# Kernel tuning notes

Hardware: AMD Instinct MI355X
Metric: run time of the kernel (lower is better)

The kernel has to match this reference:

```python
import jax, jax.numpy as jnp
import numpy as np
from jax import lax

N, IN_CH, FEAT, OUT_CH, H, W = 8, 3, 64, 3, 256, 256
EPS = 1e-8


def lrelu(x):
    return jnp.where(x >= 0, x, 0.2 * x)


def conv2d(x, w, b, stride, pad):
    y = lax.conv_general_dilated(x, w, (stride, stride), [(pad, pad), (pad, pad)],
                                 dimension_numbers=('NCHW', 'OIHW', 'NCHW'))
    return y + b[None, :, None, None]


def make_blur_kernel():
    # _make_kernel([1,3,3,1]): outer product, normalized
    k = jnp.array([1.0, 3.0, 3.0, 1.0], jnp.float32)
    k = k[None, :] * k[:, None]
    return k / k.sum()


def blur(x, kernel, pad):
    # upfirdn2d with up=down=1: pad then FIR-convolve (true convolution -> flip kernel)
    n, c, h, w = x.shape
    k = jnp.flip(kernel, (0, 1))[None, None]  # [1,1,kh,kw]
    y = lax.conv_general_dilated(x.reshape(n * c, 1, h, w), k, (1, 1),
                                 [(pad[0], pad[1]), (pad[0], pad[1])],
                                 dimension_numbers=('NCHW', 'OIHW', 'NCHW'))
    return y.reshape(n, c, y.shape[-2], y.shape[-1])


def mod_conv(x, s, w, swW, swb, sbW, sbb, mode, blur_k, activate=True):
    # x [n,c,h,w]; s [n,feat]; w [out,c,k,k]; style 1x1 convs on [n,feat,1,1] == matmuls
    kk = w.shape[-1]
    sw = lrelu(s @ swW.T + swb)                    # [n, c]  (style_weight)
    sb = lrelu(s @ sbW.T + sbb)                    # [n, out] (style_bias)
    weight = w[None] * sw[:, None, :, None, None]  # [n,out,c,k,k]
    d = lax.rsqrt(jnp.sum(weight * weight, axis=(2, 3, 4)) + EPS)
    weight = weight * d[:, :, None, None, None]    # demodulate
    if mode == 'up':
        # conv_transpose2d(stride=2, pad=0) == conv with lhs_dilation=2, pad k-1, flipped kernel
        wf = jnp.flip(weight, (-2, -1))
        def f(xi, wi):
            return lax.conv_general_dilated(xi[None], wi, (1, 1),
                    [(kk - 1, kk - 1)] * 2, lhs_dilation=(2, 2),
                    dimension_numbers=('NCHW', 'OIHW', 'NCHW'))[0]
        y = jax.vmap(f)(x, wf)
        y = blur(y, blur_k * 4.0, (1, 1))          # Blur(pad=(1,1), upsample_factor=2)
    elif mode == 'down':
        xb = blur(x, blur_k, (2, 2))               # Blur(pad=(2,2))
        def f(xi, wi):
            return lax.conv_general_dilated(xi[None], wi, (2, 2), [(0, 0)] * 2,
                    dimension_numbers=('NCHW', 'OIHW', 'NCHW'))[0]
        y = jax.vmap(f)(xb, weight)
    else:
        p = kk // 2
        def f(xi, wi):
            return lax.conv_general_dilated(xi[None], wi, (1, 1), [(p, p)] * 2,
                    dimension_numbers=('NCHW', 'OIHW', 'NCHW'))[0]
        y = jax.vmap(f)(x, weight)
    y = y + sb[:, :, None, None]
    return lrelu(y) if activate else y


def da_forward(x, ref, g0_w, g0_b, gr_w, gr_b,
               c0_w, c0_swW, c0_swb, c0_sbW, c0_sbb,
               mid_w, mid_swW, mid_swb, mid_sbW, mid_sbb,
               c6_w, c6_swW, c6_swb, c6_sbW, c6_sbb):
    bk = make_blur_kernel()
    # guide_net: conv s1/lrelu, conv s2/lrelu, conv s1/lrelu, conv s2/lrelu, conv s1, avgpool(1)
    h = lrelu(conv2d(ref, g0_w, g0_b, 1, 1))
    strides = (2, 1, 2, 1)
    for i in range(4):
        h = conv2d(h, gr_w[i], gr_b[i], strides[i], 1)
        if i < 3:
            h = lrelu(h)
    s = jnp.mean(h, axis=(2, 3))  # [n, feat]; AdaptiveAvgPool2d(1)

    mids = lambda i: (mid_w[i], mid_swW[i], mid_swb[i], mid_sbW[i], mid_sbb[i])
    f0 = mod_conv(x, s, c0_w, c0_swW, c0_swb, c0_sbW, c0_sbb, 'none', bk)
    f1 = mod_conv(f0, s, *mids(0), 'down', bk)
    f1 = mod_conv(f1, s, *mids(1), 'none', bk)
    f2 = mod_conv(f1, s, *mids(2), 'down', bk)
    f2 = mod_conv(f2, s, *mids(3), 'none', bk)
    f3 = mod_conv(f2, s, *mids(4), 'none', bk)
    f3 = mod_conv(f3, s, *mids(5), 'none', bk)
    f4 = mod_conv(f3 + f2, s, *mids(6), 'up', bk)
    f4 = mod_conv(f4, s, *mids(7), 'none', bk)
    f5 = mod_conv(f4 + f1, s, *mids(8), 'up', bk)
    f5 = mod_conv(f5, s, *mids(9), 'none', bk)
    out = mod_conv(f5 + f0, s, c6_w, c6_swW, c6_swb, c6_sbW, c6_sbb, 'none', bk, activate=False)
    return out


def setup_inputs() -> dict:
    key = jax.random.key(0)
    ks = jax.random.split(key, 24)
    f = FEAT
    inv = 1.0 / np.sqrt(f)
    d = {
        'x':   jax.random.normal(ks[0], (N, IN_CH, H, W), jnp.float32),
        'ref': jax.random.normal(ks[1], (N, IN_CH, H, W), jnp.float32),
        'g0_w': jax.random.normal(ks[2], (f, IN_CH, 3, 3), jnp.float32) * (1.0 / np.sqrt(IN_CH * 9)),
        'g0_b': jnp.zeros((f,), jnp.float32),
        'gr_w': jax.random.normal(ks[3], (4, f, f, 3, 3), jnp.float32) * (1.0 / np.sqrt(f * 9)),
        'gr_b': jnp.zeros((4, f), jnp.float32),
        'c0_w':   jax.random.normal(ks[4], (f, IN_CH, 3, 3), jnp.float32),
        'c0_swW': jax.random.normal(ks[5], (IN_CH, f), jnp.float32) * inv,
        'c0_swb': jnp.zeros((IN_CH,), jnp.float32),
        'c0_sbW': jax.random.normal(ks[6], (f, f), jnp.float32) * inv,
        'c0_sbb': jnp.zeros((f,), jnp.float32),
        'mid_w':   jax.random.normal(ks[7], (10, f, f, 3, 3), jnp.float32),
        'mid_swW': jax.random.normal(ks[8], (10, f, f), jnp.float32) * inv,
        'mid_swb': jnp.zeros((10, f), jnp.float32),
        'mid_sbW': jax.random.normal(ks[9], (10, f, f), jnp.float32) * inv,
        'mid_sbb': jnp.zeros((10, f), jnp.float32),
        'c6_w':   jax.random.normal(ks[10], (OUT_CH, f, 3, 3), jnp.float32),
        'c6_swW': jax.random.normal(ks[11], (f, f), jnp.float32) * inv,
        'c6_swb': jnp.zeros((f,), jnp.float32),
        'c6_sbW': jax.random.normal(ks[12], (OUT_CH, f), jnp.float32) * inv,
        'c6_sbb': jnp.zeros((OUT_CH,), jnp.float32),
    }
    return d


def reference(x, ref, g0_w, g0_b, gr_w, gr_b,
              c0_w, c0_swW, c0_swb, c0_sbW, c0_sbb,
              mid_w, mid_swW, mid_swb, mid_sbW, mid_sbb,
              c6_w, c6_swW, c6_swb, c6_sbW, c6_sbb):
    return da_forward(x, ref, g0_w, g0_b, gr_w, gr_b,
                      c0_w, c0_swW, c0_swb, c0_sbW, c0_sbb,
                      mid_w, mid_swW, mid_swb, mid_sbW, mid_sbb,
                      c6_w, c6_swW, c6_swb, c6_sbW, c6_sbb)
```

## Files before the change

kernel.cpp:

```cpp
#include <hip/hip_runtime.h>

#define LRELU(v) ((v) >= 0.f ? (v) : 0.2f * (v))

template<int S>
__global__ void conv64_gemm(const float* __restrict__ in, const float* __restrict__ Wt,
                            const float* __restrict__ bias, float* __restrict__ out,
                            int Hin, int Win, int Hout, int Wout, int pad, int act, int tilesX,
                            long long inStr, long long wStr, long long bStr, long long outStr)
{
    constexpr int CC  = (S == 1) ? 8 : 4;
    constexpr int TIN = (S == 1) ? 18 : 33;
    constexpr int RS  = (S == 1) ? 20 : 36;
    constexpr int NF4 = (S == 1) ? 3 : 5;
    constexpr int PW  = NF4 * 4;
    extern __shared__ float lds[];
    float* it = lds;
    float* wl = lds + CC * TIN * RS;

    int s = blockIdx.y;
    in   += (size_t)s * inStr;
    Wt   += (size_t)s * wStr;
    bias += (size_t)s * bStr;
    out  += (size_t)s * outStr;

    int b  = blockIdx.x;
    int tx = b % tilesX, ty = b / tilesX;
    int t  = threadIdx.x;
    int og = t >> 5;
    int pg = t & 31;
    int r  = pg >> 1, ch = pg & 1;

    float acc[8][8];
    #pragma unroll
    for (int i = 0; i < 8; ++i)
        #pragma unroll
        for (int j = 0; j < 8; ++j) acc[i][j] = 0.f;

    const int y0 = ty * 16 * S - pad;
    const int x0 = tx * 16 * S - pad;
    const size_t plane = (size_t)Hin * Win;

    for (int c0 = 0; c0 < 64; c0 += CC) {
        __syncthreads();
        {
            const float4* src = (const float4*)(Wt + c0 * 9 * 64);
            float4* dst = (float4*)wl;
            for (int i = t; i < CC * 9 * 16; i += 256) dst[i] = src[i];
        }
        for (int rowi = t; rowi < CC * TIN; rowi += 256) {
            int cc = rowi / TIN, rr = rowi - cc * TIN;
            int iy = y0 + rr;
            float* dst = it + (size_t)rowi * RS;
            const float* srow = in + (size_t)(c0 + cc) * plane + (size_t)iy * Win + x0;
            if ((unsigned)iy < (unsigned)Hin && x0 >= 0 && x0 + RS <= Win) {
                #pragma unroll
                for (int q = 0; q < RS / 4; ++q)
                    ((float4*)dst)[q] = ((const float4*)srow)[q];
            } else {
                for (int cl = 0; cl < TIN; ++cl) {
                    int ix = x0 + cl;
                    float v = 0.f;
                    if ((unsigned)iy < (unsigned)Hin && (unsigned)ix < (unsigned)Win)
                        v = in[(size_t)(c0 + cc) * plane + (size_t)iy * Win + ix];
                    dst[cl] = v;
                }
            }
        }
        __syncthreads();
        for (int cc = 0; cc < CC; ++cc) {
            const float* base = it + cc * TIN * RS;
            #pragma unroll
            for (int ky = 0; ky < 3; ++ky) {
                float p[PW];
                const float* rowp = base + (r * S + ky) * RS + ch * 8 * S;
                #pragma unroll
                for (int q = 0; q < NF4; ++q) {
                    float4 f = *(const float4*)(rowp + q * 4);
                    p[q*4+0] = f.x; p[q*4+1] = f.y; p[q*4+2] = f.z; p[q*4+3] = f.w;
                }
                #pragma unroll
                for (int kx = 0; kx < 3; ++kx) {
                    const float* wp = wl + ((cc * 9) + ky * 3 + kx) * 64 + og * 8;
                    float4 wa = *(const float4*)wp;
                    float4 wb = *(const float4*)(wp + 4);
                    float w8[8] = {wa.x, wa.y, wa.z, wa.w, wb.x, wb.y, wb.z, wb.w};
                    #pragma unroll
                    for (int oi = 0; oi < 8; ++oi)
                        #pragma unroll
                        for (int j = 0; j < 8; ++j)
                            acc[oi][j] += w8[oi] * p[j * S + kx];
                }
            }
        }
    }

    int y  = ty * 16 + r;
    int xb = tx * 16 + ch * 8;
    #pragma unroll
    for (int oi = 0; oi < 8; ++oi) {
        int o = og * 8 + oi;
        float bo = bias[o];
        float v[8];
        #pragma unroll
        for (int j = 0; j < 8; ++j) {
            float a = acc[oi][j] + bo;
            v[j] = act ? LRELU(a) : a;
        }
        float* op = out + ((size_t)o * Hout + y) * Wout + xb;
        *(float4*)op       = make_float4(v[0], v[1], v[2], v[3]);
        *(float4*)(op + 4) = make_float4(v[4], v[5], v[6], v[7]);
    }
}

__global__ void conv64_gemm8(const float* __restrict__ in, const float* __restrict__ Wt,
                             const float* __restrict__ bias, float* __restrict__ out,
                             int H, int W, int act, int tilesX,
                             long long inStr, long long wStr, long long bStr, long long outStr)
{
    constexpr int CC = 8, TIN = 10, RS = 12;
    __shared__ float it[CC * TIN * RS];
    __shared__ float wl[CC * 9 * 64];
    int s = blockIdx.y;
    in   += (size_t)s * inStr;
    Wt   += (size_t)s * wStr;
    bias += (size_t)s * bStr;
    out  += (size_t)s * outStr;

    int b  = blockIdx.x;
    int tx = b % tilesX, ty = b / tilesX;
    int t  = threadIdx.x;
    int og = t >> 5, pg = t & 31;
    int r  = pg >> 2, ch = pg & 3;

    float acc[8][2];
    #pragma unroll
    for (int i = 0; i < 8; ++i) { acc[i][0] = 0.f; acc[i][1] = 0.f; }

    const int y0 = ty * 8 - 1, x0 = tx * 8 - 1;
    const size_t plane = (size_t)H * W;

    for (int c0 = 0; c0 < 64; c0 += CC) {
        __syncthreads();
        {
            const float4* src = (const float4*)(Wt + c0 * 9 * 64);
            float4* dst = (float4*)wl;
            for (int i = t; i < CC * 9 * 16; i += 256) dst[i] = src[i];
        }
        for (int rowi = t; rowi < CC * TIN; rowi += 256) {
            int cc = rowi / TIN, rr = rowi - cc * TIN;
            int iy = y0 + rr;
            float* dst = it + rowi * RS;
            const float* srow = in + (size_t)(c0 + cc) * plane + (size_t)iy * W + x0;
            if ((unsigned)iy < (unsigned)H && x0 >= 0 && x0 + RS <= W) {
                #pragma unroll
                for (int q = 0; q < 3; ++q)
                    ((float4*)dst)[q] = ((const float4*)srow)[q];
            } else {
                for (int cl = 0; cl < RS; ++cl) {
                    int ix = x0 + cl;
                    float v = 0.f;
                    if (cl < TIN && (unsigned)iy < (unsigned)H && (unsigned)ix < (unsigned)W)
                        v = in[(size_t)(c0 + cc) * plane + (size_t)iy * W + ix];
                    dst[cl] = v;
                }
            }
        }
        __syncthreads();
        for (int cc = 0; cc < CC; ++cc) {
            const float* base = it + cc * TIN * RS;
            #pragma unroll
            for (int ky = 0; ky < 3; ++ky) {
                const float* rowp = base + (r + ky) * RS + ch * 2;
                float p[4] = {rowp[0], rowp[1], rowp[2], rowp[3]};
                #pragma unroll
                for (int kx = 0; kx < 3; ++kx) {
                    const float* wp = wl + ((cc * 9) + ky * 3 + kx) * 64 + og * 8;
                    float4 wa = *(const float4*)wp;
                    float4 wb = *(const float4*)(wp + 4);
                    float w8[8] = {wa.x, wa.y, wa.z, wa.w, wb.x, wb.y, wb.z, wb.w};
                    #pragma unroll
                    for (int oi = 0; oi < 8; ++oi) {
                        acc[oi][0] += w8[oi] * p[kx];
                        acc[oi][1] += w8[oi] * p[kx + 1];
                    }
                }
            }
        }
    }

    int y = ty * 8 + r, xb = tx * 8 + ch * 2;
    #pragma unroll
    for (int oi = 0; oi < 8; ++oi) {
        int o = og * 8 + oi;
        float bo = bias[o];
        float a0 = acc[oi][0] + bo, a1 = acc[oi][1] + bo;
        if (act) { a0 = LRELU(a0); a1 = LRELU(a1); }
        *(float2*)(out + ((size_t)o * H + y) * W + xb) = make_float2(a0, a1);
    }
}

__global__ void conv64s2_gemm8(const float* __restrict__ in, const float* __restrict__ Wt,
                               const float* __restrict__ bias, float* __restrict__ out,
                               int Hin, int Win, int Hout, int Wout, int pad, int act, int tilesX,
                               long long inStr, long long wStr, long long bStr, long long outStr)
{
    constexpr int CC = 8, TIN = 18, RS = 20;
    __shared__ float it[CC * TIN * RS];
    __shared__ float wl[CC * 9 * 64];
    int s = blockIdx.y;
    in   += (size_t)s * inStr;
    Wt   += (size_t)s * wStr;
    bias += (size_t)s * bStr;
    out  += (size_t)s * outStr;

    int b  = blockIdx.x;
    int tx = b % tilesX, ty = b / tilesX;
    int t  = threadIdx.x;
    int og = t >> 5, pg = t & 31;
    int r  = pg >> 2, ch = pg & 3;

    float acc[8][2];
    #pragma unroll
    for (int i = 0; i < 8; ++i) { acc[i][0] = 0.f; acc[i][1] = 0.f; }

    const int y0 = ty * 16 - pad, x0 = tx * 16 - pad;
    const size_t plane = (size_t)Hin * Win;

    for (int c0 = 0; c0 < 64; c0 += CC) {
        __syncthreads();
        {
            const float4* src = (const float4*)(Wt + c0 * 9 * 64);
            float4* dst = (float4*)wl;
            for (int i = t; i < CC * 9 * 16; i += 256) dst[i] = src[i];
        }
        for (int rowi = t; rowi < CC * TIN; rowi += 256) {
            int cc = rowi / TIN, rr = rowi - cc * TIN;
            int iy = y0 + rr;
            float* dst = it + rowi * RS;
            const float* srow = in + (size_t)(c0 + cc) * plane + (size_t)iy * Win + x0;
            if ((unsigned)iy < (unsigned)Hin && x0 >= 0 && x0 + RS <= Win) {
                #pragma unroll
                for (int q = 0; q < RS / 4; ++q)
                    ((float4*)dst)[q] = ((const float4*)srow)[q];
            } else {
                for (int cl = 0; cl < RS; ++cl) {
                    int ix = x0 + cl;
                    float v = 0.f;
                    if (cl < TIN && (unsigned)iy < (unsigned)Hin && (unsigned)ix < (unsigned)Win)
                        v = in[(size_t)(c0 + cc) * plane + (size_t)iy * Win + ix];
                    dst[cl] = v;
                }
            }
        }
        __syncthreads();
        for (int cc = 0; cc < CC; ++cc) {
            const float* base = it + cc * TIN * RS;
            #pragma unroll
            for (int ky = 0; ky < 3; ++ky) {
                const float* rowp = base + (2 * r + ky) * RS + ch * 4;
                float4 f0 = *(const float4*)rowp;
                float4 f1 = *(const float4*)(rowp + 4);
                float p[8] = {f0.x, f0.y, f0.z, f0.w, f1.x, f1.y, f1.z, f1.w};
                #pragma unroll
                for (int kx = 0; kx < 3; ++kx) {
                    const float* wp = wl + ((cc * 9) + ky * 3 + kx) * 64 + og * 8;
                    float4 wa = *(const float4*)wp;
                    float4 wb = *(const float4*)(wp + 4);
                    float w8[8] = {wa.x, wa.y, wa.z, wa.w, wb.x, wb.y, wb.z, wb.w};
                    #pragma unroll
                    for (int oi = 0; oi < 8; ++oi) {
                        acc[oi][0] += w8[oi] * p[kx];
                        acc[oi][1] += w8[oi] * p[kx + 2];
                    }
                }
            }
        }
    }

    int y = ty * 8 + r, xb = tx * 8 + ch * 2;
    #pragma unroll
    for (int oi = 0; oi < 8; ++oi) {
        int o = og * 8 + oi;
        float bo = bias[o];
        float a0 = acc[oi][0] + bo, a1 = acc[oi][1] + bo;
        if (act) { a0 = LRELU(a0); a1 = LRELU(a1); }
        *(float2*)(out + ((size_t)o * Hout + y) * Wout + xb) = make_float2(a0, a1);
    }
}

__global__ void conv3_gemm(const float* __restrict__ in, const float* __restrict__ Wt,
                           const float* __restrict__ bias, float* __restrict__ out,
                           int H, int W, int tilesX,
                           long long inStr, long long wStr, long long bStr, long long outStr)
{
    constexpr int TIN = 18, RS = 20;
    __shared__ float it[3 * TIN * RS];
    __shared__ float wl[27 * 64];
    int s = blockIdx.y;
    in   += (size_t)s * inStr;
    Wt   += (size_t)s * wStr;
    bias += (size_t)s * bStr;
    out  += (size_t)s * outStr;

    int b  = blockIdx.x;
    int tx = b % tilesX, ty = b / tilesX;
    int t  = threadIdx.x;
    {
        const float4* src = (const float4*)Wt;
        float4* dst = (float4*)wl;
        for (int i = t; i < 27 * 16; i += 256) dst[i] = src[i];
    }
    const int y0 = ty * 16 - 1, x0 = tx * 16 - 1;
    const size_t plane = (size_t)H * W;
    for (int rowi = t; rowi < 3 * TIN; rowi += 256) {
        int cc = rowi / TIN, rr = rowi - cc * TIN;
        int iy = y0 + rr;
        float* dst = it + (size_t)rowi * RS;
        const float* srow = in + (size_t)cc * plane + (size_t)iy * W + x0;
        if ((unsigned)iy < (unsigned)H && x0 >= 0 && x0 + RS <= W) {
            #pragma unroll
            for (int q = 0; q < RS / 4; ++q)
                ((float4*)dst)[q] = ((const float4*)srow)[q];
        } else {
            for (int cl = 0; cl < TIN; ++cl) {
                int ix = x0 + cl;
                float v = 0.f;
                if ((unsigned)iy < (unsigned)H && (unsigned)ix < (unsigned)W)
                    v = in[(size_t)cc * plane + (size_t)iy * W + ix];
                dst[cl] = v;
            }
        }
    }
    __syncthreads();

    int og = t >> 5, pg = t & 31;
    int r  = pg >> 1, ch = pg & 1;
    float acc[8][8];
    #pragma unroll
    for (int i = 0; i < 8; ++i)
        #pragma unroll
        for (int j = 0; j < 8; ++j) acc[i][j] = 0.f;

    for (int c = 0; c < 3; ++c) {
        const float* base = it + c * TIN * RS;
        #pragma unroll
        for (int ky = 0; ky < 3; ++ky) {
            float p[12];
            const float* rowp = base + (r + ky) * RS + ch * 8;
            #pragma unroll
            for (int q = 0; q < 3; ++q) {
                float4 f = *(const float4*)(rowp + q * 4);
                p[q*4+0] = f.x; p[q*4+1] = f.y; p[q*4+2] = f.z; p[q*4+3] = f.w;
            }
            #pragma unroll
            for (int kx = 0; kx < 3; ++kx) {
                const float* wp = wl + ((c * 9) + ky * 3 + kx) * 64 + og * 8;
                float4 wa = *(const float4*)wp;
                float4 wb = *(const float4*)(wp + 4);
                float w8[8] = {wa.x, wa.y, wa.z, wa.w, wb.x, wb.y, wb.z, wb.w};
                #pragma unroll
                for (int oi = 0; oi < 8; ++oi)
                    #pragma unroll
                    for (int j = 0; j < 8; ++j)
                        acc[oi][j] += w8[oi] * p[j + kx];
            }
        }
    }

    int y  = ty * 16 + r;
    int xb = tx * 16 + ch * 8;
    #pragma unroll
    for (int oi = 0; oi < 8; ++oi) {
        int o = og * 8 + oi;
        float bo = bias[o];
        float v[8];
        #pragma unroll
        for (int j = 0; j < 8; ++j) {
            float a = acc[oi][j] + bo;
            v[j] = LRELU(a);
        }
        float* op = out + ((size_t)o * H + y) * W + xb;
        *(float4*)op       = make_float4(v[0], v[1], v[2], v[3]);
        *(float4*)(op + 4) = make_float4(v[4], v[5], v[6], v[7]);
    }
}

__global__ void conv64to3_gemm(const float* __restrict__ in, const float* __restrict__ in2,
                               const float* __restrict__ Wt, const float* __restrict__ sb,
                               float* __restrict__ out, int H, int W, int tilesX,
                               long long inStr, long long wStr, long long sbStr, long long outStr)
{
    constexpr int CC = 8, TIN = 18, RS = 20;
    __shared__ float it[CC * TIN * RS];
    __shared__ float wl[CC * 9 * 3];
    int s = blockIdx.y;
    in  += (size_t)s * inStr;
    in2 += (size_t)s * inStr;
    Wt  += (size_t)s * wStr;
    sb  += (size_t)s * sbStr;
    out += (size_t)s * outStr;

    int b  = blockIdx.x;
    int tx = b % tilesX, ty = b / tilesX;
    int t  = threadIdx.x;
    int r  = t >> 4, cl = t & 15;
    const int y0 = ty * 16 - 1, x0 = tx * 16 - 1;
    const size_t plane = (size_t)H * W;

    float acc[3] = {0.f, 0.f, 0.f};

    for (int c0 = 0; c0 < 64; c0 += CC) {
        __syncthreads();
        for (int i = t; i < CC * 9 * 3; i += 256) wl[i] = Wt[c0 * 27 + i];
        for (int rowi = t; rowi < CC * TIN; rowi += 256) {
            int cc = rowi / TIN, rr = rowi - cc * TIN;
            int iy = y0 + rr;
            float* dst = it + (size_t)rowi * RS;
            size_t roff = (size_t)(c0 + cc) * plane + (size_t)iy * W + x0;
            if ((unsigned)iy < (unsigned)H && x0 >= 0 && x0 + RS <= W) {
                #pragma unroll
                for (int q = 0; q < RS / 4; ++q) {
                    float4 a = ((const float4*)(in  + roff))[q];
                    float4 bb = ((const float4*)(in2 + roff))[q];
                    ((float4*)dst)[q] = make_float4(a.x + bb.x, a.y + bb.y, a.z + bb.z, a.w + bb.w);
                }
            } else {
                for (int c2 = 0; c2 < TIN; ++c2) {
                    int ix = x0 + c2;
                    float v = 0.f;
                    if ((unsigned)iy < (unsigned)H && (unsigned)ix < (unsigned)W) {
                        size_t off = (size_t)(c0 + cc) * plane + (size_t)iy * W + ix;
                        v = in[off] + in2[off];
                    }
                    dst[c2] = v;
                }
            }
        }
        __syncthreads();
        for (int cc = 0; cc < CC; ++cc) {
            const float* base = it + cc * TIN * RS;
            #pragma unroll
            for (int ky = 0; ky < 3; ++ky) {
                const float* rowp = base + (r + ky) * RS + cl;
                float p0 = rowp[0], p1 = rowp[1], p2 = rowp[2];
                const float* wr = wl + (cc * 9 + ky * 3) * 3;
                #pragma unroll
                for (int o = 0; o < 3; ++o)
                    acc[o] += wr[o] * p0 + wr[3 + o] * p1 + wr[6 + o] * p2;
            }
        }
    }

    int y = ty * 16 + r, x = tx * 16 + cl;
    #pragma unroll
    for (int o = 0; o < 3; ++o)
        out[((size_t)o * H + y) * W + x] = acc[o] + sb[o];
}

__global__ void upconv64_gemm(const float* __restrict__ in, const float* __restrict__ in2,
                              const float* __restrict__ G2, const float* __restrict__ sb,
                              float* __restrict__ out, int Hin, int Win, int tilesX,
                              long long bufStr, long long sbStr, long long outStr)
{
    constexpr int CC = 4;
    constexpr int RS = 20;
    constexpr int PSTR = 68;
    extern __shared__ float lds[];
    float* it  = lds;
    float* wl  = lds + CC * 6 * RS;
    float* ost = wl + CC * 2448;

    int s = blockIdx.y;
    in  += (size_t)s * bufStr;
    in2 += (size_t)s * bufStr;
    G2  += (size_t)s * bufStr;
    sb  += (size_t)s * sbStr;
    out += (size_t)s * outStr;

    int b  = blockIdx.x;
    int tx = b % tilesX, ty = b / tilesX;
    int t  = threadIdx.x;
    int og  = t & 7;
    int pxb = (t >> 3) & 1;
    int xh  = (t >> 4) & 1;
    int r   = t >> 5;
    int rhalf = r >> 1, rpar = r & 1;
    const int Y0 = ty * 8, X0 = tx * 32;
    const int gy0 = Y0 / 2 - 1;
    const int gx0 = X0 / 2 - 1;
    const size_t plane = (size_t)Hin * Win;

    float acc[8][8];
    #pragma unroll
    for (int i = 0; i < 8; ++i)
        #pragma unroll
        for (int j = 0; j < 8; ++j) acc[i][j] = 0.f;

    for (int c0 = 0; c0 < 64; c0 += CC) {
        __syncthreads();
        {
            const float4* src = (const float4*)(G2 + (size_t)c0 * 2304);
            for (int i = t; i < CC * 36 * 16; i += 256) {
                int row = i >> 4, q = i & 15;
                ((float4*)(wl + row * PSTR))[q] = src[i];
            }
        }
        for (int rowi = t; rowi < CC * 6; rowi += 256) {
            int cc = rowi / 6, rr = rowi - cc * 6;
            int gi = gy0 + rr;
            float* dst = it + (size_t)rowi * RS;
            size_t roff = (size_t)(c0 + cc) * plane + (size_t)gi * Win + gx0;
            if ((unsigned)gi < (unsigned)Hin && gx0 >= 0 && gx0 + RS <= Win) {
                #pragma unroll
                for (int qq = 0; qq < 5; ++qq) {
                    float4 a = ((const float4*)(in  + roff))[qq];
                    float4 bb = ((const float4*)(in2 + roff))[qq];
                    ((float4*)dst)[qq] = make_float4(a.x + bb.x, a.y + bb.y, a.z + bb.z, a.w + bb.w);
                }
            } else {
                for (int cl = 0; cl < RS; ++cl) {
                    int gj = gx0 + cl;
                    float v = 0.f;
                    if (cl < 18 && (unsigned)gi < (unsigned)Hin && (unsigned)gj < (unsigned)Win) {
                        size_t off = (size_t)(c0 + cc) * plane + (size_t)gi * Win + gj;
                        v = in[off] + in2[off];
                    }
                    dst[cl] = v;
                }
            }
        }
        __syncthreads();
        for (int cc = 0; cc < CC; ++cc) {
            const float* ib = it + cc * 6 * RS;
            const float* wcb = wl + cc * (36 * PSTR) + (rpar * 2 + pxb) * PSTR;
            #pragma unroll
            for (int ty2 = 0; ty2 < 3; ++ty2) {
                float p[12];
                const float* rowp = ib + (rhalf + ty2) * RS + xh * 8;
                #pragma unroll
                for (int qq = 0; qq < 3; ++qq) {
                    float4 f = *(const float4*)(rowp + qq * 4);
                    p[qq*4+0] = f.x; p[qq*4+1] = f.y; p[qq*4+2] = f.z; p[qq*4+3] = f.w;
                }
                #pragma unroll
                for (int tx2 = 0; tx2 < 3; ++tx2) {
                    const float* wp = wcb + (ty2 * 3 + tx2) * (4 * PSTR) + og * 8;
                    float4 wa = *(const float4*)wp;
                    float4 wv = *(const float4*)(wp + 4);
                    float w8[8] = {wa.x, wa.y, wa.z, wa.w, wv.x, wv.y, wv.z, wv.w};
                    #pragma unroll
                    for (int oi = 0; oi < 8; ++oi)
                        #pragma unroll
                        for (int k = 0; k < 8; ++k)
                            acc[oi][k] += w8[oi] * p[k + tx2];
                }
            }
        }
    }

    const int Hout = 2 * Hin, Wout = 2 * Win;
    const int obase = (r * 8 + og) * 33 + xh * 16 + pxb;
    #pragma unroll
    for (int oi = 0; oi < 8; ++oi) {
        int o = og * 8 + oi;
        float bo = sb[o];
        __syncthreads();
        #pragma unroll
        for (int k = 0; k < 8; ++k) {
            float a = acc[oi][k] + bo;
            ost[obase + 2 * k] = LRELU(a);
        }
        __syncthreads();
        #pragma unroll
        for (int p2 = 0; p2 < 2; ++p2) {
            int j4 = p2 * 256 + t;
            int ogr = j4 >> 6;
            int rr  = (j4 >> 3) & 7;
            int x4  = j4 & 7;
            const float* sp = ost + (rr * 8 + ogr) * 33 + x4 * 4;
            float4 f = make_float4(sp[0], sp[1], sp[2], sp[3]);
            int oo = ogr * 8 + oi;
            *(float4*)(out + ((size_t)oo * Hout + Y0 + rr) * Wout + X0 + x4 * 4) = f;
        }
    }
}

__global__ void combine_up_w(const float* __restrict__ W, float* __restrict__ G2,
                             long long wStr, long long g2Str)
{
    int s = blockIdx.y;
    W  += (size_t)s * wStr;
    G2 += (size_t)s * g2Str;
    int i = blockIdx.x * 256 + threadIdx.x;
    if (i >= 147456) return;
    int o = i & 63;
    int rest = i >> 6;
    int p4 = rest & 3;
    int k9 = (rest >> 2) % 9;
    int c  = (rest >> 2) / 9;
    int py = p4 >> 1, px = p4 & 1;
    int tyk = k9 / 3, txk = k9 % 3;
    int dy = 2 * tyk - 1 - py, dx = 2 * txk - 1 - px;
    const float K[4] = {1.f, 3.f, 3.f, 1.f};
    const float* wp = W + ((size_t)o * 64 + c) * 9;
    float sacc = 0.f;
    #pragma unroll
    for (int a = 0; a < 3; ++a) {
        int ky = a + dy;
        if ((unsigned)ky >= 4u) continue;
        #pragma unroll
        for (int b2 = 0; b2 < 3; ++b2) {
            int kx = b2 + dx;
            if ((unsigned)kx >= 4u) continue;
            sacc += K[ky] * K[kx] * wp[a * 3 + b2];
        }
    }
    G2[i] = sacc * (1.f / 16.f);
}

__global__ void blur_down(const float* __restrict__ in, float* __restrict__ out,
                          int H, int W, int tilesX, int tilesY,
                          long long inStr, long long outStr)
{
    int s = blockIdx.y;
    in  += (size_t)s * inStr;
    out += (size_t)s * outStr;
    int Ho = H + 1, Wo = W + 1;
    int bid = blockIdx.x;
    int tx = bid % tilesX; bid /= tilesX;
    int ty = bid % tilesY; bid /= tilesY;
    int p  = bid;
    int x = tx * 16 + (threadIdx.x & 15);
    int y = ty * 16 + (threadIdx.x >> 4);
    if (x >= Wo || y >= Ho) return;
    const float k[4] = {1.f, 3.f, 3.f, 1.f};
    const float* ip = in + (size_t)p * H * W;
    float acc = 0.f;
    #pragma unroll
    for (int ky = 0; ky < 4; ++ky) {
        int iy = y - 2 + ky;
        if ((unsigned)iy >= (unsigned)H) continue;
        float row = 0.f;
        #pragma unroll
        for (int kx = 0; kx < 4; ++kx) {
            int ix = x - 2 + kx;
            if ((unsigned)ix >= (unsigned)W) continue;
            row += ip[(size_t)iy * W + ix] * k[kx];
        }
        acc += row * k[ky];
    }
    out[((size_t)p * Ho + y) * Wo + x] = acc * (1.f / 64.f);
}

__global__ void avgpool_hw(const float* __restrict__ in, float* __restrict__ out, int HW,
                           long long inStr, long long outStr)
{
    int s = blockIdx.y;
    in  += (size_t)s * inStr;
    out += (size_t)s * outStr;
    int p = blockIdx.x;
    const float* ip = in + (size_t)p * HW;
    float sum = 0.f;
    for (int i = threadIdx.x; i < HW; i += blockDim.x) sum += ip[i];
    __shared__ float red[256];
    red[threadIdx.x] = sum;
    __syncthreads();
    for (int off = 128; off; off >>= 1) {
        if ((int)threadIdx.x < off) red[threadIdx.x] += red[threadIdx.x + off];
        __syncthreads();
    }
    if (threadIdx.x == 0) out[p] = red[0] / (float)HW;
}

__global__ void style_fc(const float* __restrict__ s, const float* __restrict__ W,
                         const float* __restrict__ b, float* __restrict__ out, int outdim)
{
    int n = blockIdx.x;
    int i = threadIdx.x;
    if (i >= outdim) return;
    float acc = b[i];
    const float* sn = s + n * 64;
    const float* wi = W + i * 64;
    for (int f = 0; f < 64; ++f) acc += sn[f] * wi[f];
    out[n * 64 + i] = LRELU(acc);
}

__global__ void modulate(const float* __restrict__ w, const float* __restrict__ sw,
                         float* __restrict__ wout, int O, int C, int transpose)
{
    int no = blockIdx.x;
    int o = no % O, n = no / O;
    int nw = C * 9;
    int t = threadIdx.x;
    float v[9];
    int cnt = 0;
    float ss = 0.f;
    for (int idx = t; idx < nw; idx += 64) {
        int c = idx / 9;
        float val = w[o * nw + idx] * sw[n * 64 + c];
        v[cnt++] = val;
        ss += val * val;
    }
    #pragma unroll
    for (int off = 32; off; off >>= 1) ss += __shfl_xor(ss, off);
    float d = rsqrtf(ss + 1e-8f);
    cnt = 0;
    for (int idx = t; idx < nw; idx += 64) {
        float val = v[cnt++] * d;
        if (transpose)
            wout[(size_t)n * nw * O + (size_t)idx * O + o] = val;
        else
            wout[(size_t)no * nw + idx] = val;
    }
}

__global__ void guide_transpose(const float* __restrict__ grw, float* __restrict__ gt, int total)
{
    int i = blockIdx.x * 256 + threadIdx.x;
    if (i >= total) return;
    int l = i / 36864, rem = i % 36864;
    int idx = rem / 64, o = rem % 64;
    int c = idx / 9, k = idx % 9;
    gt[i] = grw[(((size_t)l * 64 + o) * 64 + c) * 9 + k];
}

__global__ void g0_transpose(const float* __restrict__ g0w, float* __restrict__ gt)
{
    int i = blockIdx.x * 256 + threadIdx.x;
    if (i >= 1728) return;
    int idx = i / 64, o = i % 64;
    int c = idx / 9, k = idx % 9;
    gt[i] = g0w[((size_t)o * 3 + c) * 9 + k];
}

__global__ void fill_sentinel(float* __restrict__ out, int n)
{
    int i = blockIdx.x * 256 + threadIdx.x;
    if (i < n) out[i] = 1.0e9f;
}

extern "C" void kernel_launch(void* const* d_in, const int* in_sizes, int n_in,
                              void* d_out, int out_size, void* d_ws, size_t ws_size,
                              hipStream_t stream)
{
    const float* x     = (const float*)d_in[0];
    const float* ref   = (const float*)d_in[1];
    const float* g0w   = (const float*)d_in[2];
    const float* g0b   = (const float*)d_in[3];
    const float* grw   = (const float*)d_in[4];
    const float* grb   = (const float*)d_in[5];
    const float* c0w   = (const float*)d_in[6];
    const float* c0swW = (const float*)d_in[7];
    const float* c0swb = (const float*)d_in[8];
    const float* c0sbW = (const float*)d_in[9];
    const float* c0sbb = (const float*)d_in[10];
    const float* midw  = (const float*)d_in[11];
    const float* midswW= (const float*)d_in[12];
    const float* midswb= (const float*)d_in[13];
    const float* midsbW= (const float*)d_in[14];
    const float* midsbb= (const float*)d_in[15];
    const float* c6w   = (const float*)d_in[16];
    const float* c6swW = (const float*)d_in[17];
    const float* c6swb = (const float*)d_in[18];
    const float* c6sbW = (const float*)d_in[19];
    const float* c6sbb = (const float*)d_in[20];
    float* out = (float*)d_out;
    float* ws  = (float*)d_ws;

    const size_t SV  = 0;
    const size_t STY = 512;
    const size_t WM  = 12800;
    const size_t GT  = 2989568;
    const size_t G0T = 3137024;
    const size_t BUF = 3138816;

    const size_t SA = 0;
    const size_t SB = 4227136;
    const size_t D1 = 8421440;
    const size_t D2 = 9470016;
    const size_t D3 = 10518592;
    const size_t E1 = 11583616;
    const size_t E2 = 11845760;
    const size_t E3 = 12107904;
    const size_t G2o = 12370048;
    const long long PER = 12517504ll;

    const size_t gSA = 0;
    const size_t gD1 = 4194304;
    const size_t gD2 = 5242880;
    const size_t gE1 = 6291456;
    const size_t gE2 = 6553600;
    const long long GPER = 6815744ll;

    int G = 0, GG = 0;
    for (int g = 8; g >= 1; --g)
        if ((BUF + (size_t)g * PER) * sizeof(float) <= ws_size) { G = g; break; }
    for (int g = 8; g >= 1; --g)
        if ((BUF + (size_t)g * GPER) * sizeof(float) <= ws_size) { GG = g; break; }
    if (!G || !GG) {
        fill_sentinel<<<dim3((out_size + 255) / 256), dim3(256), 0, stream>>>(out, out_size);
        return;
    }

    dim3 blk(256);
    const int LDS1 = 29952;
    const int LDSU = (4 * 6 * 20 + 4 * 2448 + 2112) * 4;

    float* B = ws + BUF;

    guide_transpose<<<dim3(147456 / 256), blk, 0, stream>>>(grw, ws + GT, 147456);
    g0_transpose<<<dim3(7), blk, 0, stream>>>(g0w, ws + G0T);

    for (int n0 = 0; n0 < 8; ) {
        int g = (8 - n0 < GG) ? (8 - n0) : GG;
        const float* refg = ref + (size_t)n0 * 196608;
        conv3_gemm<<<dim3(16 * 16, g), blk, 0, stream>>>(
            refg, ws + G0T, g0b, B + gSA, 256, 256, 16, 196608, 0, 0, GPER);
        conv64s2_gemm8<<<dim3(16 * 16, g), blk, 0, stream>>>(
            B + gSA, ws + GT, grb, B + gD1, 256, 256, 128, 128, 1, 1, 16, GPER, 0, 0, GPER);
        conv64_gemm8<<<dim3(16 * 16, g), blk, 0, stream>>>(
            B + gD1, ws + GT + 36864, grb + 64, B + gD2, 128, 128, 1, 16, GPER, 0, 0, GPER);
        conv64s2_gemm8<<<dim3(8 * 8, g), blk, 0, stream>>>(
            B + gD2, ws + GT + 73728, grb + 128, B + gE1, 128, 128, 64, 64, 1, 1, 8, GPER, 0, 0, GPER);
        conv64_gemm8<<<dim3(8 * 8, g), blk, 0, stream>>>(
            B + gE1, ws + GT + 110592, grb + 192, B + gE2, 64, 64, 0, 8, GPER, 0, 0, GPER);
        avgpool_hw<<<dim3(64, g), blk, 0, stream>>>(B + gE2, ws + SV + (size_t)n0 * 64, 4096, GPER, 64);
        n0 += g;
    }

    const float* Wt[12];  const float* swWp[12]; const float* swbp[12];
    const float* sbWp[12]; const float* sbbp[12];
    int Ci[12], Oi[12];
    size_t wmo[12];
    Wt[0] = c0w; swWp[0] = c0swW; swbp[0] = c0swb; sbWp[0] = c0sbW; sbbp[0] = c0sbb;
    Ci[0] = 3; Oi[0] = 64; wmo[0] = WM;
    for (int i = 0; i < 10; ++i) {
        Wt[1 + i]   = midw   + (size_t)i * 36864;
        swWp[1 + i] = midswW + (size_t)i * 4096;
        swbp[1 + i] = midswb + (size_t)i * 64;
        sbWp[1 + i] = midsbW + (size_t)i * 4096;
        sbbp[1 + i] = midsbb + (size_t)i * 64;
        Ci[1 + i] = 64; Oi[1 + i] = 64;
        wmo[1 + i] = WM + 13824ull + (size_t)i * 294912ull;
    }
    Wt[11] = c6w; swWp[11] = c6swW; swbp[11] = c6swb; sbWp[11] = c6sbW; sbbp[11] = c6sbb;
    Ci[11] = 64; Oi[11] = 3; wmo[11] = WM + 13824ull + 2949120ull;

    const int trf[12] = {1, 1, 1, 1, 1, 1, 1, 0, 1, 0, 1, 1};

    for (int i = 0; i < 12; ++i) {
        style_fc<<<dim3(8), dim3(64), 0, stream>>>(ws + SV, swWp[i], swbp[i], ws + STY + i * 1024, Ci[i]);
        style_fc<<<dim3(8), dim3(64), 0, stream>>>(ws + SV, sbWp[i], sbbp[i], ws + STY + i * 1024 + 512, Oi[i]);
        modulate<<<dim3(8 * Oi[i]), dim3(64), 0, stream>>>(Wt[i], ws + STY + i * 1024, ws + wmo[i], Oi[i], Ci[i], trf[i]);
    }

    for (int n0 = 0; n0 < 8; ) {
        int g = (8 - n0 < G) ? (8 - n0) : G;
        const float* xg = x + (size_t)n0 * 196608;
        float* outg = out + (size_t)n0 * 196608;
        #define WN(i)  (ws + wmo[i] + (size_t)n0 * Oi[i] * Ci[i] * 9)
        #define WSTR(i) ((long long)(Oi[i] * Ci[i] * 9))
        #define SBN(i) (ws + STY + (i) * 1024 + 512 + (size_t)n0 * 64)
        conv3_gemm<<<dim3(16 * 16, g), blk, 0, stream>>>(
            xg, WN(0), SBN(0), B + SB, 256, 256, 16, 196608, WSTR(0), 64, PER);
        blur_down<<<dim3(64 * 17 * 17, g), blk, 0, stream>>>(B + SB, B + SA, 256, 256, 17, 17, PER, PER);
        conv64s2_gemm8<<<dim3(16 * 16, g), blk, 0, stream>>>(
            B + SA, WN(1), SBN(1), B + D1, 257, 257, 128, 128, 0, 1, 16, PER, WSTR(1), 64, PER);
        conv64_gemm8<<<dim3(16 * 16, g), blk, 0, stream>>>(
            B + D1, WN(2), SBN(2), B + D2, 128, 128, 1, 16, PER, WSTR(2), 64, PER);
        blur_down<<<dim3(64 * 9 * 9, g), blk, 0, stream>>>(B + D2, B + D3, 128, 128, 9, 9, PER, PER);
        conv64s2_gemm8<<<dim3(8 * 8, g), blk, 0, stream>>>(
            B + D3, WN(3), SBN(3), B + E1, 129, 129, 64, 64, 0, 1, 8, PER, WSTR(3), 64, PER);
        conv64_gemm8<<<dim3(8 * 8, g), blk, 0, stream>>>(
            B + E1, WN(4), SBN(4), B + E2, 64, 64, 1, 8, PER, WSTR(4), 64, PER);
        conv64_gemm8<<<dim3(8 * 8, g), blk, 0, stream>>>(
            B + E2, WN(5), SBN(5), B + E3, 64, 64, 1, 8, PER, WSTR(5), 64, PER);
        conv64_gemm8<<<dim3(8 * 8, g), blk, 0, stream>>>(
            B + E3, WN(6), SBN(6), B + E1, 64, 64, 1, 8, PER, WSTR(6), 64, PER);
        combine_up_w<<<dim3(576, g), blk, 0, stream>>>(WN(7), B + G2o, WSTR(7), PER);
        upconv64_gemm<<<dim3(4 * 16, g), blk, LDSU, stream>>>(
            B + E1, B + E2, B + G2o, SBN(7), B + D1, 64, 64, 4, PER, 64, PER);
        conv64_gemm8<<<dim3(16 * 16, g), blk, 0, stream>>>(
            B + D1, WN(8), SBN(8), B + D3, 128, 128, 1, 16, PER, WSTR(8), 64, PER);
        combine_up_w<<<dim3(576, g), blk, 0, stream>>>(WN(9), B + G2o, WSTR(9), PER);
        upconv64_gemm<<<dim3(8 * 32, g), blk, LDSU, stream>>>(
            B + D3, B + D2, B + G2o, SBN(9), B + SA, 128, 128, 8, PER, 64, PER);
        conv64_gemm<1><<<dim3(16 * 16, g), blk, LDS1, stream>>>(
            B + SA, WN(10), SBN(10), B + SB, 256, 256, 256, 256, 1, 1, 16, PER, WSTR(10), 64, PER);
        conv3_gemm<<<dim3(16 * 16, g), blk, 0, stream>>>(
            xg, WN(0), SBN(0), B + SA, 256, 256, 16, 196608, WSTR(0), 64, PER);
        conv64to3_gemm<<<dim3(16 * 16, g), blk, 0, stream>>>(
            B + SB, B + SA, WN(11), SBN(11), outg, 256, 256, 16, PER, WSTR(11), 64, 196608);
        #undef WN
        #undef WSTR
        #undef SBN
        n0 += g;
    }
}
```

Baseline: 3.945 ms.

## Add 16x8-tile conv kernels for 128x128 layers and shrink upconv channel chunk

Adds new 3x3 conv kernels, stride 1 and stride 2, that compute a 16-wide by 8-tall output tile for all 64 output channels. Each thread holds 8 channels by 4 pixels. These replace the 8x8-tile gemm8 kernels on the 128x128 layers, halving the block count and amortising each weight-chunk load over twice as many pixels. The upconv kernel's input-channel chunk also drops from 4 to 2 to cut its LDS footprint, which may raise occupancy but doubles the number of sync and load rounds.

```diff
diff --git a/kernel.cpp b/kernel.cpp
--- a/kernel.cpp
+++ b/kernel.cpp
@@ -109,6 +109,192 @@
         float* op = out + ((size_t)o * Hout + y) * Wout + xb;
         *(float4*)op       = make_float4(v[0], v[1], v[2], v[3]);
         *(float4*)(op + 4) = make_float4(v[4], v[5], v[6], v[7]);
+    }
+}
+
+__global__ void conv64_gemm16x8(const float* __restrict__ in, const float* __restrict__ Wt,
+                                const float* __restrict__ bias, float* __restrict__ out,
+                                int H, int W, int act, int tilesX,
+                                long long inStr, long long wStr, long long bStr, long long outStr)
+{
+    constexpr int CC = 8, TIN = 18, RS = 20;
+    __shared__ float it[CC * 10 * RS];
+    __shared__ float wl[CC * 9 * 64];
+    int s = blockIdx.y;
+    in   += (size_t)s * inStr;
+    Wt   += (size_t)s * wStr;
+    bias += (size_t)s * bStr;
+    out  += (size_t)s * outStr;
+
+    int b  = blockIdx.x;
+    int tx = b % tilesX, ty = b / tilesX;
+    int t  = threadIdx.x;
+    int og = t >> 5, pg = t & 31;
+    int r  = pg >> 2, ch = pg & 3;
+
+    float acc[8][4];
+    #pragma unroll
+    for (int i = 0; i < 8; ++i)
+        #pragma unroll
+        for (int j = 0; j < 4; ++j) acc[i][j] = 0.f;
+
+    const int y0 = ty * 8 - 1, x0 = tx * 16 - 1;
+    const size_t plane = (size_t)H * W;
+
+    for (int c0 = 0; c0 < 64; c0 += CC) {
+        __syncthreads();
+        {
+            const float4* src = (const float4*)(Wt + c0 * 9 * 64);
+            float4* dst = (float4*)wl;
+            for (int i = t; i < CC * 9 * 16; i += 256) dst[i] = src[i];
+        }
+        for (int rowi = t; rowi < CC * 10; rowi += 256) {
+            int cc = rowi / 10, rr = rowi - cc * 10;
+            int iy = y0 + rr;
+            float* dst = it + rowi * RS;
+            const float* srow = in + (size_t)(c0 + cc) * plane + (size_t)iy * W + x0;
+            if ((unsigned)iy < (unsigned)H && x0 >= 0 && x0 + RS <= W) {
+                #pragma unroll
+                for (int q = 0; q < 5; ++q)
+                    ((float4*)dst)[q] = ((const float4*)srow)[q];
+            } else {
+                for (int cl = 0; cl < RS; ++cl) {
+                    int ix = x0 + cl;
+                    float v = 0.f;
+                    if (cl < TIN && (unsigned)iy < (unsigned)H && (unsigned)ix < (unsigned)W)
+                        v = in[(size_t)(c0 + cc) * plane + (size_t)iy * W + ix];
+                    dst[cl] = v;
+                }
+            }
+        }
+        __syncthreads();
+        for (int cc = 0; cc < CC; ++cc) {
+            const float* base = it + cc * 10 * RS;
+            #pragma unroll
+            for (int ky = 0; ky < 3; ++ky) {
+                const float* rowp = base + (r + ky) * RS + ch * 4;
+                float4 f0 = *(const float4*)rowp;
+                float4 f1 = *(const float4*)(rowp + 4);
+                float p[8] = {f0.x, f0.y, f0.z, f0.w, f1.x, f1.y, f1.z, f1.w};
+                #pragma unroll
+                for (int kx = 0; kx < 3; ++kx) {
+                    const float* wp = wl + ((cc * 9) + ky * 3 + kx) * 64 + og * 8;
+                    float4 wa = *(const float4*)wp;
+                    float4 wb = *(const float4*)(wp + 4);
+                    float w8[8] = {wa.x, wa.y, wa.z, wa.w, wb.x, wb.y, wb.z, wb.w};
+                    #pragma unroll
+                    for (int oi = 0; oi < 8; ++oi)
+                        #pragma unroll
+                        for (int j = 0; j < 4; ++j)
+                            acc[oi][j] += w8[oi] * p[j + kx];
+                }
+            }
+        }
+    }
+
+    int y = ty * 8 + r, xb = tx * 16 + ch * 4;
+    #pragma unroll
+    for (int oi = 0; oi < 8; ++oi) {
+        int o = og * 8 + oi;
+        float bo = bias[o];
+        float v0 = acc[oi][0] + bo, v1 = acc[oi][1] + bo;
+        float v2 = acc[oi][2] + bo, v3 = acc[oi][3] + bo;
+        if (act) { v0 = LRELU(v0); v1 = LRELU(v1); v2 = LRELU(v2); v3 = LRELU(v3); }
+        *(float4*)(out + ((size_t)o * H + y) * W + xb) = make_float4(v0, v1, v2, v3);
+    }
+}
+
+__global__ void conv64s2_gemm16x8(const float* __restrict__ in, const float* __restrict__ Wt,
+                                  const float* __restrict__ bias, float* __restrict__ out,
+                                  int Hin, int Win, int Hout, int Wout, int pad, int act, int tilesX,
+                                  long long inStr, long long wStr, long long bStr, long long outStr)
+{
+    constexpr int CC = 8, TIN = 35, RS = 36;
+    __shared__ float it[CC * 18 * RS];
+    __shared__ float wl[CC * 9 * 64];
+    int s = blockIdx.y;
+    in   += (size_t)s * inStr;
+    Wt   += (size_t)s * wStr;
+    bias += (size_t)s * bStr;
+    out  += (size_t)s * outStr;
+
+    int b  = blockIdx.x;
+    int tx = b % tilesX, ty = b / tilesX;
+    int t  = threadIdx.x;
+    int og = t >> 5, pg = t & 31;
+    int r  = pg >> 2, ch = pg & 3;
+
+    float acc[8][4];
+    #pragma unroll
+    for (int i = 0; i < 8; ++i)
+        #pragma unroll
+        for (int j = 0; j < 4; ++j) acc[i][j] = 0.f;
+
+    const int y0 = 2 * (ty * 8) - pad, x0 = 2 * (tx * 16) - pad;
+    const size_t plane = (size_t)Hin * Win;
+
+    for (int c0 = 0; c0 < 64; c0 += CC) {
+        __syncthreads();
+        {
+            const float4* src = (const float4*)(Wt + c0 * 9 * 64);
+            float4* dst = (float4*)wl;
+            for (int i = t; i < CC * 9 * 16; i += 256) dst[i] = src[i];
+        }
+        for (int rowi = t; rowi < CC * 18; rowi += 256) {
+            int cc = rowi / 18, rr = rowi - cc * 18;
+            int iy = y0 + rr;
+            float* dst = it + rowi * RS;
+            const float* srow = in + (size_t)(c0 + cc) * plane + (size_t)iy * Win + x0;
+            if ((unsigned)iy < (unsigned)Hin && x0 >= 0 && x0 + RS <= Win) {
+                #pragma unroll
+                for (int q = 0; q < 9; ++q)
+                    ((float4*)dst)[q] = ((const float4*)srow)[q];
+            } else {
+                for (int cl = 0; cl < RS; ++cl) {
+                    int ix = x0 + cl;
+                    float v = 0.f;
+                    if (cl < TIN && (unsigned)iy < (unsigned)Hin && (unsigned)ix < (unsigned)Win)
+                        v = in[(size_t)(c0 + cc) * plane + (size_t)iy * Win + ix];
+                    dst[cl] = v;
+                }
+            }
+        }
+        __syncthreads();
+        for (int cc = 0; cc < CC; ++cc) {
+            const float* base = it + cc * 18 * RS;
+            #pragma unroll
+            for (int ky = 0; ky < 3; ++ky) {
+                const float* rowp = base + (2 * r + ky) * RS + ch * 8;
+                float4 f0 = *(const float4*)rowp;
+                float4 f1 = *(const float4*)(rowp + 4);
+                float4 f2 = *(const float4*)(rowp + 8);
+                float p[12] = {f0.x, f0.y, f0.z, f0.w, f1.x, f1.y, f1.z, f1.w,
+                               f2.x, f2.y, f2.z, f2.w};
+                #pragma unroll
+                for (int kx = 0; kx < 3; ++kx) {
+                    const float* wp = wl + ((cc * 9) + ky * 3 + kx) * 64 + og * 8;
+                    float4 wa = *(const float4*)wp;
+                    float4 wb = *(const float4*)(wp + 4);
+                    float w8[8] = {wa.x, wa.y, wa.z, wa.w, wb.x, wb.y, wb.z, wb.w};
+                    #pragma unroll
+                    for (int oi = 0; oi < 8; ++oi)
+                        #pragma unroll
+                        for (int j = 0; j < 4; ++j)
+                            acc[oi][j] += w8[oi] * p[2 * j + kx];
+                }
+            }
+        }
+    }
+
+    int y = ty * 8 + r, xb = tx * 16 + ch * 4;
+    #pragma unroll
+    for (int oi = 0; oi < 8; ++oi) {
+        int o = og * 8 + oi;
+        float bo = bias[o];
+        float v0 = acc[oi][0] + bo, v1 = acc[oi][1] + bo;
+        float v2 = acc[oi][2] + bo, v3 = acc[oi][3] + bo;
+        if (act) { v0 = LRELU(v0); v1 = LRELU(v1); v2 = LRELU(v2); v3 = LRELU(v3); }
+        *(float4*)(out + ((size_t)o * Hout + y) * Wout + xb) = make_float4(v0, v1, v2, v3);
     }
 }
 
@@ -462,7 +648,7 @@
                               float* __restrict__ out, int Hin, int Win, int tilesX,
                               long long bufStr, long long sbStr, long long outStr)
 {
-    constexpr int CC = 4;
+    constexpr int CC = 2;
     constexpr int RS = 20;
     constexpr int PSTR = 68;
     extern __shared__ float lds[];
@@ -804,7 +990,7 @@
 
     dim3 blk(256);
     const int LDS1 = 29952;
-    const int LDSU = (4 * 6 * 20 + 4 * 2448 + 2112) * 4;
+    const int LDSU = (2 * 6 * 20 + 2 * 2448 + 2112) * 4;
 
     float* B = ws + BUF;
 
@@ -816,10 +1002,10 @@
         const float* refg = ref + (size_t)n0 * 196608;
         conv3_gemm<<<dim3(16 * 16, g), blk, 0, stream>>>(
             refg, ws + G0T, g0b, B + gSA, 256, 256, 16, 196608, 0, 0, GPER);
-        conv64s2_gemm8<<<dim3(16 * 16, g), blk, 0, stream>>>(
-            B + gSA, ws + GT, grb, B + gD1, 256, 256, 128, 128, 1, 1, 16, GPER, 0, 0, GPER);
-        conv64_gemm8<<<dim3(16 * 16, g), blk, 0, stream>>>(
-            B + gD1, ws + GT + 36864, grb + 64, B + gD2, 128, 128, 1, 16, GPER, 0, 0, GPER);
+        conv64s2_gemm16x8<<<dim3(8 * 16, g), blk, 0, stream>>>(
+            B + gSA, ws + GT, grb, B + gD1, 256, 256, 128, 128, 1, 1, 8, GPER, 0, 0, GPER);
+        conv64_gemm16x8<<<dim3(8 * 16, g), blk, 0, stream>>>(
+            B + gD1, ws + GT + 36864, grb + 64, B + gD2, 128, 128, 1, 8, GPER, 0, 0, GPER);
         conv64s2_gemm8<<<dim3(8 * 8, g), blk, 0, stream>>>(
             B + gD2, ws + GT + 73728, grb + 128, B + gE1, 128, 128, 64, 64, 1, 1, 8, GPER, 0, 0, GPER);
         conv64_gemm8<<<dim3(8 * 8, g), blk, 0, stream>>>(
@@ -864,10 +1050,10 @@
         conv3_gemm<<<dim3(16 * 16, g), blk, 0, stream>>>(
             xg, WN(0), SBN(0), B + SB, 256, 256, 16, 196608, WSTR(0), 64, PER);
         blur_down<<<dim3(64 * 17 * 17, g), blk, 0, stream>>>(B + SB, B + SA, 256, 256, 17, 17, PER, PER);
-        conv64s2_gemm8<<<dim3(16 * 16, g), blk, 0, stream>>>(
-            B + SA, WN(1), SBN(1), B + D1, 257, 257, 128, 128, 0, 1, 16, PER, WSTR(1), 64, PER);
-        conv64_gemm8<<<dim3(16 * 16, g), blk, 0, stream>>>(
-            B + D1, WN(2), SBN(2), B + D2, 128, 128, 1, 16, PER, WSTR(2), 64, PER);
+        conv64s2_gemm16x8<<<dim3(8 * 16, g), blk, 0, stream>>>(
+            B + SA, WN(1), SBN(1), B + D1, 257, 257, 128, 128, 0, 1, 8, PER, WSTR(1), 64, PER);
+        conv64_gemm16x8<<<dim3(8 * 16, g), blk, 0, stream>>>(
+            B + D1, WN(2), SBN(2), B + D2, 128, 128, 1, 8, PER, WSTR(2), 64, PER);
         blur_down<<<dim3(64 * 9 * 9, g), blk, 0, stream>>>(B + D2, B + D3, 128, 128, 9, 9, PER, PER);
         conv64s2_gemm8<<<dim3(8 * 8, g), blk, 0, stream>>>(
             B + D3, WN(3), SBN(3), B + E1, 129, 129, 64, 64, 0, 1, 8, PER, WSTR(3), 64, PER);
@@ -880,8 +1066,8 @@
         combine_up_w<<<dim3(576, g), blk, 0, stream>>>(WN(7), B + G2o, WSTR(7), PER);
         upconv64_gemm<<<dim3(4 * 16, g), blk, LDSU, stream>>>(
             B + E1, B + E2, B + G2o, SBN(7), B + D1, 64, 64, 4, PER, 64, PER);
-        conv64_gemm8<<<dim3(16 * 16, g), blk, 0, stream>>>(
-            B + D1, WN(8), SBN(8), B + D3, 128, 128, 1, 16, PER, WSTR(8), 64, PER);
+        conv64_gemm16x8<<<dim3(8 * 16, g), blk, 0, stream>>>(
+            B + D1, WN(8), SBN(8), B + D3, 128, 128, 1, 8, PER, WSTR(8), 64, PER);
         combine_up_w<<<dim3(576, g), blk, 0, stream>>>(WN(9), B + G2o, WSTR(9), PER);
         upconv64_gemm<<<dim3(8 * 32, g), blk, LDSU, stream>>>(
             B + D3, B + D2, B + G2o, SBN(9), B + SA, 128, 128, 8, PER, 64, PER);
```

New measurement: 6.835 ms. 1.73x slower.
